# Kernel optimization log

Measured on AMD Instinct MI355X. Metric: run time of the kernel, lower is better.

The kernel has to match this reference:

```python
import jax, jax.numpy as jnp
import numpy as np
from jax import lax


def setup_inputs() -> dict:
    key = jax.random.key(0)
    x = jax.random.normal(key, (32, 1024, 2048), dtype=jnp.float32)
    return {"x": x}


def reference(x):
    # x: [B, F, T] trellis of per-(frame, token) scores.
    # Recurrence: out[:, i+1, j] = x[:, i+1, j] + softtruemax(out[:, i, j], out[:, i, j-1])
    # where the j-1 candidate is -inf for j == 0 (then hard max -> out[:, i, 0]).
    # softtruemax of two finite values a, b with temperature 1:
    #   w = softmax([a, b]); value = w_a*a + w_b*b, and w_a = sigmoid(a - b).
    def step(carry, xrow):
        a = carry                                   # stay:    out[:, i, j]
        b = jnp.pad(carry[:, :-1], ((0, 0), (1, 0)))  # advance: out[:, i, j-1] (j=0 slot overridden below)
        p = jax.nn.sigmoid(a - b)                   # softmax weight on `a`
        soft = p * a + (1.0 - p) * b
        vals = soft.at[:, 0].set(a[:, 0])           # j=0: -inf candidate -> hard max = a
        new = xrow + vals
        return new, new

    first = x[:, 0, :]                               # [B, T]
    xs = jnp.moveaxis(x[:, 1:, :], 1, 0)             # [F-1, B, T]
    _, rows = lax.scan(step, first, xs)              # rows: [F-1, B, T]
    out = jnp.concatenate([first[None], rows], axis=0)  # [F, B, T]
    return jnp.moveaxis(out, 0, 1)                   # [B, F, T]
```

## Files before the change

### kernel.cpp

```cpp
#include <hip/hip_runtime.h>


#define TT  1024
#define DD  2048
#define BLK 64
#define DPX 16
#define DPB 8

__device__ __forceinline__ float softstep(float a, float bl) {
    float d = a - bl;
    float p = __builtin_amdgcn_rcpf(1.0f + __expf(-d));
    return fmaf(p, d, bl);
}

template<int NC>
__global__ __launch_bounds__(BLK, 1)
void softscan_kernel(const float* __restrict__ x, float* __restrict__ out,
                     unsigned long long* __restrict__ slots)
{
    constexpr int VPT = DD / NC / BLK;
    typedef float vecN __attribute__((ext_vector_type(VPT)));

    const int b    = blockIdx.x;
    const int k    = blockIdx.y;
    const int lane = threadIdx.x;
    const int c0   = k * (BLK * VPT) + lane * VPT;
    const int strideV = DD / VPT;

    const vecN* __restrict__ xp = (const vecN*)(x + (size_t)b * TT * DD + c0);
    vecN* __restrict__ op       = (vecN*)(out + (size_t)b * TT * DD + c0);

    unsigned long long* pubSlot =
        slots + ((size_t)b * (NC - 1) + k) * TT;
    const unsigned long long* rdSlot =
        slots + ((size_t)b * (NC - 1) + (k - 1)) * TT;

    vecN carry = xp[0];
    __builtin_nontemporal_store(carry, &op[0]);

    float xleft0 = 0.0f;
    if (k > 0 && lane == 0) xleft0 = x[(size_t)b * TT * DD + (c0 - 1)];

    vecN xbuf[DPX];
    unsigned long long bbuf[DPB];
#pragma unroll
    for (int s = 0; s < DPX; ++s)
        xbuf[s] = xp[(size_t)(s + 1) * strideV];
    if (k > 0 && lane == 0) {
#pragma unroll
        for (int s = 1; s < DPB; ++s)
            bbuf[s] = __hip_atomic_load(&rdSlot[s], __ATOMIC_RELAXED,
                                        __HIP_MEMORY_SCOPE_AGENT);
    }

#define STEP_BODY(S_, J_, PF_X_)                                              \
    {                                                                         \
        const int s = (S_);                                                   \
        const int t = s + 1;                                                  \
        vecN xv = xbuf[(J_)];                                                 \
        float leftv = 0.0f;                                                   \
        if (k > 0 && lane == 0) {                                             \
            if (s == 0) leftv = xleft0;                                       \
            else {                                                            \
                unsigned long long raw = bbuf[(J_) & (DPB - 1)];              \
                while ((unsigned)(raw >> 32) != (unsigned)s)                  \
                    raw = __hip_atomic_load(&rdSlot[s], __ATOMIC_RELAXED,     \
                                            __HIP_MEMORY_SCOPE_AGENT);        \
                leftv = __uint_as_float((unsigned)raw);                       \
            }                                                                 \
        }                                                                     \
        float sh   = __shfl_up(carry[VPT - 1], 1);                            \
        float left = (lane == 0) ? leftv : sh;                                \
        vecN n;                                                               \
        float s0 = softstep(carry[0], left);                                  \
        n[0] = xv[0] + ((k == 0 && lane == 0) ? carry[0] : s0);               \
        _Pragma("unroll")                                                     \
        for (int i = 1; i < VPT; ++i)                                         \
            n[i] = xv[i] + softstep(carry[i], carry[i - 1]);                  \
        carry = n;                                                            \
        __builtin_nontemporal_store(carry, &op[(size_t)t * strideV]);         \
        if (k < NC - 1 && lane == BLK - 1 && t <= TT - 2) {                   \
            unsigned long long pk =                                           \
                ((unsigned long long)(unsigned)t << 32) |                     \
                (unsigned long long)__float_as_uint(carry[VPT - 1]);          \
            __hip_atomic_store(&pubSlot[t], pk, __ATOMIC_RELAXED,             \
                               __HIP_MEMORY_SCOPE_AGENT);                     \
        }                                                                     \
        if (PF_X_) {                                                          \
            int row = s + DPX + 1; if (row > TT - 1) row = TT - 1;            \
            xbuf[(J_)] = xp[(size_t)row * strideV];                           \
        }                                                                     \
        const int spb = s + DPB;                                              \
        if (k > 0 && lane == 0 && spb <= TT - 2)                              \
            bbuf[(J_) & (DPB - 1)] =                                          \
                __hip_atomic_load(&rdSlot[spb], __ATOMIC_RELAXED,             \
                                  __HIP_MEMORY_SCOPE_AGENT);                  \
    }

    for (int m = 0; m < (TT - 1) / DPX; ++m) {
#pragma unroll
        for (int j = 0; j < DPX; ++j)
            STEP_BODY(m * DPX + j, j, true)
    }
#pragma unroll
    for (int e = 0; e < (TT - 1) % DPX; ++e)
        STEP_BODY(((TT - 1) / DPX) * DPX + e, e, false)

#undef STEP_BODY
}

__global__ __launch_bounds__(BLK, 1)
void softscan_fallback(const float* __restrict__ x, float* __restrict__ out)
{
    constexpr int VPT = DD / BLK;
    const int b    = blockIdx.x;
    const int lane = threadIdx.x;
    const int c0   = lane * VPT;

    const float* __restrict__ xp = x + (size_t)b * TT * DD + c0;
    float* __restrict__ op       = out + (size_t)b * TT * DD + c0;

    float carry[VPT];
#pragma unroll
    for (int i = 0; i < VPT; ++i) carry[i] = xp[i];
#pragma unroll
    for (int i = 0; i < VPT; ++i) op[i] = carry[i];

    for (int t = 1; t < TT; ++t) {
        const float* xr = xp + (size_t)t * DD;
        float* orow     = op + (size_t)t * DD;
        float xv[VPT];
#pragma unroll
        for (int i = 0; i < VPT; ++i) xv[i] = xr[i];

        float sh   = __shfl_up(carry[VPT - 1], 1);
        float n0;
        if (lane == 0) n0 = xv[0] + carry[0];
        else           n0 = xv[0] + softstep(carry[0], sh);
        float n[VPT];
        n[0] = n0;
#pragma unroll
        for (int i = 1; i < VPT; ++i)
            n[i] = xv[i] + softstep(carry[i], carry[i - 1]);
#pragma unroll
        for (int i = 0; i < VPT; ++i) { carry[i] = n[i]; orow[i] = n[i]; }
    }
}

extern "C" void kernel_launch(void* const* d_in, const int* in_sizes, int n_in,
                              void* d_out, int out_size, void* d_ws, size_t ws_size,
                              hipStream_t stream) {
    const float* x = (const float*)d_in[0];
    float* out = (float*)d_out;
    unsigned long long* slots = (unsigned long long*)d_ws;
    const size_t need16 = (size_t)32 * 15 * TT * sizeof(unsigned long long);
    const size_t need8  = (size_t)32 * 7  * TT * sizeof(unsigned long long);
    if (d_ws != nullptr && ws_size >= need16) {
        softscan_kernel<16><<<dim3(32, 16), dim3(BLK), 0, stream>>>(x, out, slots);
    } else if (d_ws != nullptr && ws_size >= need8) {
        softscan_kernel<8><<<dim3(32, 8), dim3(BLK), 0, stream>>>(x, out, slots);
    } else {
        softscan_fallback<<<dim3(32), dim3(BLK), 0, stream>>>(x, out);
    }
}
```

Before: 684.1 us.

## Stream x rows into an LDS ring via direct global-to-LDS loads

Adds a new kernel for the 16-chunk path that prefetches input rows into a 32-deep shared-memory ring using global_load_lds, paired two rows per issue, with explicit vmcnt waits. It also swaps the shuffle for a DPP row shift and deepens the neighbor-slot prefetch to 16. The goal is to hide global load latency on the serial recurrence without holding a large register buffer. The cost is complex manual waitcnt accounting, where a miscounted wait could read stale LDS data. The DPP row_shr also may not cross 16-lane rows.

Measured after the change: 1.039 ms. +51.8%, slower.

```diff
diff --git a/kernel.cpp b/kernel.cpp
--- a/kernel.cpp
+++ b/kernel.cpp
@@ -1,16 +1,162 @@
 #include <hip/hip_runtime.h>
 
 
-#define TT  1024
-#define DD  2048
-#define BLK 64
-#define DPX 16
-#define DPB 8
+#define TT   1024
+#define DD   2048
+#define BLK  64
+#define NCQ  16
+#define VPT  2
+#define CPC  (BLK*VPT)
+#define RP   32
+#define NPAIR 512
+#define DPB  16
+
+typedef float v2f __attribute__((ext_vector_type(2)));
 
 __device__ __forceinline__ float softstep(float a, float bl) {
     float d = a - bl;
     float p = __builtin_amdgcn_rcpf(1.0f + __expf(-d));
     return fmaf(p, d, bl);
+}
+
+__device__ __forceinline__ float wave_shr1(float v) {
+    int i = __builtin_amdgcn_update_dpp(__float_as_int(v), __float_as_int(v),
+                                        0x138 , 0xF, 0xF, false);
+    return __int_as_float(i);
+}
+
+__global__ __launch_bounds__(BLK, 1)
+void softscan_lds(const float* __restrict__ x, float* __restrict__ out,
+                  unsigned long long* __restrict__ slots)
+{
+    const int b    = blockIdx.x;
+    const int k    = blockIdx.y;
+    const int lane = threadIdx.x;
+    const size_t xbase = (size_t)b * TT * DD;
+    const int c0   = k * CPC + lane * VPT;
+    const int colg = k * CPC + (lane & 31) * 4;
+
+    v2f* op2 = (v2f*)(out + xbase + c0);
+
+    unsigned long long* pubSlot =
+        slots + ((size_t)b * (NCQ - 1) + k) * TT;
+    const unsigned long long* rdSlot =
+        slots + ((size_t)b * (NCQ - 1) + (k - 1)) * TT;
+
+    __shared__ float ring[RP * 256];
+
+    v2f carry = *(const v2f*)(x + xbase + c0);
+    __builtin_nontemporal_store(carry, &op2[0]);
+
+    float xleft0 = 0.0f;
+    if (k > 0 && lane == 0) xleft0 = x[xbase + c0 - 1];
+
+#define ISSUE_PAIR(Q_)                                                        \
+    {                                                                         \
+        const int q_ = (Q_);                                                  \
+        int ra_ = 2 * q_ + 1 + (lane >> 5);                                   \
+        if (ra_ > TT - 1) ra_ = TT - 1;                                       \
+        const float* g_ = x + xbase + (size_t)ra_ * DD + colg;                \
+        __builtin_amdgcn_global_load_lds(                                     \
+            (const __attribute__((address_space(1))) void*)g_,                \
+            (__attribute__((address_space(3))) void*)&ring[(q_ & (RP-1))*256],\
+            16, 0, 0);                                                        \
+    }
+
+#define READ_PAIR(Q_, A_, B_)                                                 \
+    {                                                                         \
+        const float* lb_ = &ring[((Q_) & (RP - 1)) * 256 + lane * 2];         \
+        A_ = *(const v2f*)lb_;                                                \
+        B_ = *(const v2f*)(lb_ + 128);                                        \
+    }
+
+    unsigned long long bbuf[DPB];
+
+#pragma unroll
+    for (int q = 0; q < RP; ++q) ISSUE_PAIR(q)
+    if (k > 0 && lane == 0) {
+#pragma unroll
+        for (int s = 1; s < DPB; ++s)
+            bbuf[s] = __hip_atomic_load(&rdSlot[s], __ATOMIC_RELAXED,
+                                        __HIP_MEMORY_SCOPE_AGENT);
+    }
+    asm volatile("s_waitcnt vmcnt(0)" ::: "memory");
+
+    v2f xc0, xc1, xn0, xn1;
+    READ_PAIR(0, xc0, xc1)
+    READ_PAIR(1, xn0, xn1)
+
+#define DOSTEP(S_, JS_, XV_)                                                  \
+    {                                                                         \
+        const int s_ = (S_);                                                  \
+        const int t_ = s_ + 1;                                                \
+        float leftv_ = 0.0f;                                                  \
+        if (k > 0 && lane == 0) {                                             \
+            if (s_ == 0) leftv_ = xleft0;                                     \
+            else {                                                            \
+                unsigned long long raw_ = bbuf[(JS_)];                        \
+                while ((unsigned)(raw_ >> 32) != (unsigned)s_)                \
+                    raw_ = __hip_atomic_load(&rdSlot[s_], __ATOMIC_RELAXED,   \
+                                             __HIP_MEMORY_SCOPE_AGENT);       \
+                leftv_ = __uint_as_float((unsigned)raw_);                     \
+            }                                                                 \
+        }                                                                     \
+        float sh_   = wave_shr1(carry.y);                                     \
+        float left_ = (lane == 0) ? leftv_ : sh_;                             \
+        float n0_ = (XV_).x + ((k == 0 && lane == 0)                          \
+                                   ? carry.x : softstep(carry.x, left_));     \
+        float n1_ = (XV_).y + softstep(carry.y, carry.x);                     \
+        carry.x = n0_; carry.y = n1_;                                         \
+        __builtin_nontemporal_store(carry, &op2[(size_t)t_ * (DD / VPT)]);    \
+        if (k < NCQ - 1 && lane == BLK - 1 && t_ <= TT - 2) {                 \
+            unsigned long long pk_ =                                          \
+                ((unsigned long long)(unsigned)t_ << 32) |                    \
+                (unsigned long long)__float_as_uint(n1_);                     \
+            __hip_atomic_store(&pubSlot[t_], pk_, __ATOMIC_RELAXED,           \
+                               __HIP_MEMORY_SCOPE_AGENT);                     \
+        }                                                                     \
+        const int spb_ = s_ + DPB;                                            \
+        if (k > 0 && lane == 0 && spb_ <= TT - 2)                             \
+            bbuf[(JS_)] = __hip_atomic_load(&rdSlot[spb_], __ATOMIC_RELAXED,  \
+                                            __HIP_MEMORY_SCOPE_AGENT);        \
+    }
+
+    int p = 0;
+    for (int m = 0; m < 63; ++m) {
+#pragma unroll
+        for (int j = 0; j < 8; ++j) {
+            const int s0 = 2 * p;
+            DOSTEP(s0,     2 * j,     xc0)
+            DOSTEP(s0 + 1, 2 * j + 1, xc1)
+            if (p + RP < NPAIR) ISSUE_PAIR(p + RP)
+            asm volatile("s_waitcnt vmcnt(48)" ::: "memory");
+            int pr = p + 2; if (pr > NPAIR - 1) pr = NPAIR - 1;
+            v2f a0, a1; READ_PAIR(pr, a0, a1)
+            xc0 = xn0; xc1 = xn1; xn0 = a0; xn1 = a1;
+            ++p;
+        }
+    }
+#pragma unroll
+    for (int e = 0; e < 7; ++e) {
+        const int s0 = 2 * (504 + e);
+        DOSTEP(s0,     2 * e,     xc0)
+        DOSTEP(s0 + 1, 2 * e + 1, xc1)
+        asm volatile("s_waitcnt vmcnt(48)" ::: "memory");
+        int pr = 504 + e + 2; if (pr > NPAIR - 1) pr = NPAIR - 1;
+        v2f a0, a1; READ_PAIR(pr, a0, a1)
+        xc0 = xn0; xc1 = xn1; xn0 = a0; xn1 = a1;
+    }
+    DOSTEP(1022, 14, xc0)
+
+#undef DOSTEP
+#undef READ_PAIR
+#undef ISSUE_PAIR
+}
+
+#define DPX 16
+
+__device__ __forceinline__ float softstep_legacy(float a, float bl) {
+    return softstep(a, bl);
 }
 
 template<int NC>
@@ -18,14 +164,14 @@
 void softscan_kernel(const float* __restrict__ x, float* __restrict__ out,
                      unsigned long long* __restrict__ slots)
 {
-    constexpr int VPT = DD / NC / BLK;
-    typedef float vecN __attribute__((ext_vector_type(VPT)));
+    constexpr int VPTL = DD / NC / BLK;
+    typedef float vecN __attribute__((ext_vector_type(VPTL)));
 
     const int b    = blockIdx.x;
     const int k    = blockIdx.y;
     const int lane = threadIdx.x;
-    const int c0   = k * (BLK * VPT) + lane * VPT;
-    const int strideV = DD / VPT;
+    const int c0   = k * (BLK * VPTL) + lane * VPTL;
+    const int strideV = DD / VPTL;
 
     const vecN* __restrict__ xp = (const vecN*)(x + (size_t)b * TT * DD + c0);
     vecN* __restrict__ op       = (vecN*)(out + (size_t)b * TT * DD + c0);
@@ -42,13 +188,13 @@
     if (k > 0 && lane == 0) xleft0 = x[(size_t)b * TT * DD + (c0 - 1)];
 
     vecN xbuf[DPX];
-    unsigned long long bbuf[DPB];
+    unsigned long long bbuf[8];
 #pragma unroll
     for (int s = 0; s < DPX; ++s)
         xbuf[s] = xp[(size_t)(s + 1) * strideV];
     if (k > 0 && lane == 0) {
 #pragma unroll
-        for (int s = 1; s < DPB; ++s)
+        for (int s = 1; s < 8; ++s)
             bbuf[s] = __hip_atomic_load(&rdSlot[s], __ATOMIC_RELAXED,
                                         __HIP_MEMORY_SCOPE_AGENT);
     }
@@ -62,27 +208,27 @@
         if (k > 0 && lane == 0) {                                             \
             if (s == 0) leftv = xleft0;                                       \
             else {                                                            \
-                unsigned long long raw = bbuf[(J_) & (DPB - 1)];              \
+                unsigned long long raw = bbuf[(J_) & 7];                      \
                 while ((unsigned)(raw >> 32) != (unsigned)s)                  \
                     raw = __hip_atomic_load(&rdSlot[s], __ATOMIC_RELAXED,     \
                                             __HIP_MEMORY_SCOPE_AGENT);        \
                 leftv = __uint_as_float((unsigned)raw);                       \
             }                                                                 \
         }                                                                     \
-        float sh   = __shfl_up(carry[VPT - 1], 1);                            \
+        float sh   = __shfl_up(carry[VPTL - 1], 1);                           \
         float left = (lane == 0) ? leftv : sh;                                \
         vecN n;                                                               \
         float s0 = softstep(carry[0], left);                                  \
         n[0] = xv[0] + ((k == 0 && lane == 0) ? carry[0] : s0);               \
         _Pragma("unroll")                                                     \
-        for (int i = 1; i < VPT; ++i)                                         \
+        for (int i = 1; i < VPTL; ++i)                                        \
             n[i] = xv[i] + softstep(carry[i], carry[i - 1]);                  \
         carry = n;                                                            \
         __builtin_nontemporal_store(carry, &op[(size_t)t * strideV]);         \
         if (k < NC - 1 && lane == BLK - 1 && t <= TT - 2) {                   \
             unsigned long long pk =                                           \
                 ((unsigned long long)(unsigned)t << 32) |                     \
-                (unsigned long long)__float_as_uint(carry[VPT - 1]);          \
+                (unsigned long long)__float_as_uint(carry[VPTL - 1]);         \
             __hip_atomic_store(&pubSlot[t], pk, __ATOMIC_RELAXED,             \
                                __HIP_MEMORY_SCOPE_AGENT);                     \
         }                                                                     \
@@ -90,9 +236,9 @@
             int row = s + DPX + 1; if (row > TT - 1) row = TT - 1;            \
             xbuf[(J_)] = xp[(size_t)row * strideV];                           \
         }                                                                     \
-        const int spb = s + DPB;                                              \
+        const int spb = s + 8;                                                \
         if (k > 0 && lane == 0 && spb <= TT - 2)                              \
-            bbuf[(J_) & (DPB - 1)] =                                          \
+            bbuf[(J_) & 7] =                                                  \
                 __hip_atomic_load(&rdSlot[spb], __ATOMIC_RELAXED,             \
                                   __HIP_MEMORY_SCOPE_AGENT);                  \
     }
@@ -112,38 +258,36 @@
 __global__ __launch_bounds__(BLK, 1)
 void softscan_fallback(const float* __restrict__ x, float* __restrict__ out)
 {
-    constexpr int VPT = DD / BLK;
+    constexpr int VPTF = DD / BLK;
     const int b    = blockIdx.x;
     const int lane = threadIdx.x;
-    const int c0   = lane * VPT;
+    const int c0   = lane * VPTF;
 
     const float* __restrict__ xp = x + (size_t)b * TT * DD + c0;
     float* __restrict__ op       = out + (size_t)b * TT * DD + c0;
 
-    float carry[VPT];
-#pragma unroll
-    for (int i = 0; i < VPT; ++i) carry[i] = xp[i];
-#pragma unroll
-    for (int i = 0; i < VPT; ++i) op[i] = carry[i];
+    float carry[VPTF];
+#pragma unroll
+    for (int i = 0; i < VPTF; ++i) carry[i] = xp[i];
+#pragma unroll
+    for (int i = 0; i < VPTF; ++i) op[i] = carry[i];
 
     for (int t = 1; t < TT; ++t) {
         const float* xr = xp + (size_t)t * DD;
         float* orow     = op + (size_t)t * DD;
-        float xv[VPT];
-#pragma unroll
-        for (int i = 0; i < VPT; ++i) xv[i] = xr[i];
-
-        float sh   = __shfl_up(carry[VPT - 1], 1);
-        float n0;
-        if (lane == 0) n0 = xv[0] + carry[0];
-        else           n0 = xv[0] + softstep(carry[0], sh);
-        float n[VPT];
-        n[0] = n0;
-#pragma unroll
-        for (int i = 1; i < VPT; ++i)
+        float xv[VPTF];
+#pragma unroll
+        for (int i = 0; i < VPTF; ++i) xv[i] = xr[i];
+
+        float sh = __shfl_up(carry[VPTF - 1], 1);
+        float n[VPTF];
+        if (lane == 0) n[0] = xv[0] + carry[0];
+        else           n[0] = xv[0] + softstep(carry[0], sh);
+#pragma unroll
+        for (int i = 1; i < VPTF; ++i)
             n[i] = xv[i] + softstep(carry[i], carry[i - 1]);
 #pragma unroll
-        for (int i = 0; i < VPT; ++i) { carry[i] = n[i]; orow[i] = n[i]; }
+        for (int i = 0; i < VPTF; ++i) { carry[i] = n[i]; orow[i] = n[i]; }
     }
 }
 
@@ -156,7 +300,7 @@
     const size_t need16 = (size_t)32 * 15 * TT * sizeof(unsigned long long);
     const size_t need8  = (size_t)32 * 7  * TT * sizeof(unsigned long long);
     if (d_ws != nullptr && ws_size >= need16) {
-        softscan_kernel<16><<<dim3(32, 16), dim3(BLK), 0, stream>>>(x, out, slots);
+        softscan_lds<<<dim3(32, NCQ), dim3(BLK), 0, stream>>>(x, out, slots);
     } else if (d_ws != nullptr && ws_size >= need8) {
         softscan_kernel<8><<<dim3(32, 8), dim3(BLK), 0, stream>>>(x, out, slots);
     } else {
```
